# Kernel tuning notes

Measured on AMD Instinct MI355X. Metric: run time of the kernel, lower is better.

## Reference

```python
import jax, jax.numpy as jnp
import numpy as np

N_LOC = 500000
N_CAT = 5000
N_EDGES = 2000000
LOC_DIM = 128
CAT_DIM = 128
INITRANGE = 0.1
NEG_SLOPE = 0.2


def setup_inputs() -> dict:
    key = jax.random.key(0)
    k1, k2, k3, k4 = jax.random.split(key, 4)
    loc_emb = jax.random.normal(k1, (N_LOC, LOC_DIM), dtype=jnp.float32)
    # loc_to_cat Linear params, init per init_weights(): uniform(-0.1, 0.1) weight, zero bias
    W = jax.random.uniform(k2, (CAT_DIM, LOC_DIM), dtype=jnp.float32,
                           minval=-INITRANGE, maxval=INITRANGE)
    b = jnp.zeros((CAT_DIM,), dtype=jnp.float32)
    edge_src = jax.random.randint(k3, (N_EDGES,), 0, N_LOC, dtype=jnp.int64)
    edge_dst = jax.random.randint(k4, (N_EDGES,), 0, N_CAT, dtype=jnp.int64)
    return {"loc_emb": loc_emb, "W": W, "b": b,
            "edge_src": edge_src, "edge_dst": edge_dst}


def reference(loc_emb, W, b, edge_src, edge_dst):
    # copy_u('f','m') + sum('m','in') across all canonical etypes, combined with 'sum':
    # gather source (loc) features along edges, segment-sum into cat nodes.
    msg = loc_emb[edge_src]                                   # [E, loc_dim]
    agg = jax.ops.segment_sum(msg, edge_dst, num_segments=N_CAT)  # [n_cat, loc_dim]
    # loc_to_cat linear + LeakyReLU(0.2)
    cat_emb = jax.nn.leaky_relu(agg @ W.T + b, negative_slope=NEG_SLOPE)
    return cat_emb
```

## Files before the change

kernel.cpp:

```cpp
#include <hip/hip_runtime.h>

#define N_LOC   500000
#define N_CAT   5000
#define N_EDGES 2000000
#define DIM     128
#define NEG_SLOPE 0.2f
#define PAD     5008
#define NB      256
#define EPB     ((N_EDGES + NB - 1) / NB)


__launch_bounds__(1024)
__global__ void blockhist_kernel(const int* __restrict__ edst, int* __restrict__ rank,
                                 int* __restrict__ bhist) {
    __shared__ int lh[N_CAT];
    int b = blockIdx.x, t = threadIdx.x;
    for (int c = t; c < N_CAT; c += 1024) lh[c] = 0;
    __syncthreads();
    int s = b * EPB;
    int e = min(s + EPB, N_EDGES);
    for (int i = s + t; i < e; i += 1024)
        rank[i] = atomicAdd(&lh[edst[i]], 1);
    __syncthreads();
    for (int c = t; c < N_CAT; c += 1024)
        bhist[(size_t)b * N_CAT + c] = lh[c];
}

__launch_bounds__(256)
__global__ void blockscan_kernel(int* __restrict__ bhist, int* __restrict__ tot) {
    int c = blockIdx.x * 256 + threadIdx.x;
    if (c >= N_CAT) return;
    int run = 0;
    for (int b0 = 0; b0 < NB; b0 += 8) {
        int v0 = bhist[(size_t)(b0 + 0) * N_CAT + c];
        int v1 = bhist[(size_t)(b0 + 1) * N_CAT + c];
        int v2 = bhist[(size_t)(b0 + 2) * N_CAT + c];
        int v3 = bhist[(size_t)(b0 + 3) * N_CAT + c];
        int v4 = bhist[(size_t)(b0 + 4) * N_CAT + c];
        int v5 = bhist[(size_t)(b0 + 5) * N_CAT + c];
        int v6 = bhist[(size_t)(b0 + 6) * N_CAT + c];
        int v7 = bhist[(size_t)(b0 + 7) * N_CAT + c];
        bhist[(size_t)(b0 + 0) * N_CAT + c] = run; run += v0;
        bhist[(size_t)(b0 + 1) * N_CAT + c] = run; run += v1;
        bhist[(size_t)(b0 + 2) * N_CAT + c] = run; run += v2;
        bhist[(size_t)(b0 + 3) * N_CAT + c] = run; run += v3;
        bhist[(size_t)(b0 + 4) * N_CAT + c] = run; run += v4;
        bhist[(size_t)(b0 + 5) * N_CAT + c] = run; run += v5;
        bhist[(size_t)(b0 + 6) * N_CAT + c] = run; run += v6;
        bhist[(size_t)(b0 + 7) * N_CAT + c] = run; run += v7;
    }
    tot[c] = run;
}

__launch_bounds__(1024)
__global__ void scan_kernel(const int* __restrict__ cnt, int* __restrict__ offsets) {
    __shared__ int wsum[16];
    __shared__ int woff[16];
    __shared__ int total_s;
    __shared__ int running_s;
    int t = threadIdx.x;
    int lane = t & 63, w = t >> 6;
    if (t == 0) { running_s = 0; offsets[0] = 0; }
    __syncthreads();
    for (int base = 0; base < N_CAT; base += 1024) {
        int i = base + t;
        int v = (i < N_CAT) ? cnt[i] : 0;
        int incl = v;
        #pragma unroll
        for (int off = 1; off < 64; off <<= 1) {
            int x = __shfl_up(incl, off, 64);
            if (lane >= off) incl += x;
        }
        if (lane == 63) wsum[w] = incl;
        __syncthreads();
        if (w == 0 && lane < 16) {
            int s = wsum[lane];
            int e = s;
            #pragma unroll
            for (int off = 1; off < 16; off <<= 1) {
                int x = __shfl_up(e, off, 64);
                if (lane >= off) e += x;
            }
            woff[lane] = e - s;
            if (lane == 15) total_s = e;
        }
        __syncthreads();
        int run = running_s;
        if (i < N_CAT) offsets[i + 1] = run + woff[w] + incl;
        __syncthreads();
        if (t == 0) running_s = run + total_s;
        __syncthreads();
    }
}

__global__ void fill2_kernel(const int* __restrict__ esrc, const int* __restrict__ edst,
                             const int* __restrict__ rank, const int* __restrict__ offsets,
                             const int* __restrict__ bhist, int* __restrict__ csr_src) {
    int i = blockIdx.x * blockDim.x + threadIdx.x;
    if (i < N_EDGES) {
        int c = edst[i];
        int b = i / EPB;
        csr_src[offsets[c] + bhist[(size_t)b * N_CAT + c] + rank[i]] = esrc[i];
    }
}

__global__ void transpose_kernel(const float* __restrict__ W, float* __restrict__ WT) {
    int j = blockIdx.x;
    int k = threadIdx.x;
    WT[k * DIM + j] = W[j * DIM + k];
}

__launch_bounds__(256)
__global__ void agg_fused_kernel(const float* __restrict__ loc, const int* __restrict__ csr_src,
                                 const int* __restrict__ offsets, const float* __restrict__ WT,
                                 const float* __restrict__ bias, float* __restrict__ out) {
    __shared__ float4 sacc[256];
    __shared__ float  srow[DIM];
    int c = blockIdx.x;
    int t = threadIdx.x;
    int g = t >> 5;
    int l = t & 31;
    int beg = offsets[c];
    int end = offsets[c + 1];
    int cnt = end - beg;
    int per = (cnt + 7) >> 3;
    int gbeg = beg + g * per;
    int gend = min(gbeg + per, end);

    float4 a0 = make_float4(0.f, 0.f, 0.f, 0.f);
    float4 a1 = make_float4(0.f, 0.f, 0.f, 0.f);
    float4 a2 = make_float4(0.f, 0.f, 0.f, 0.f);
    float4 a3 = make_float4(0.f, 0.f, 0.f, 0.f);
    int e = gbeg;
    for (; e + 4 <= gend; e += 4) {
        int s0 = csr_src[e + 0];
        int s1 = csr_src[e + 1];
        int s2 = csr_src[e + 2];
        int s3 = csr_src[e + 3];
        float4 v0 = ((const float4*)(loc + (size_t)s0 * DIM))[l];
        float4 v1 = ((const float4*)(loc + (size_t)s1 * DIM))[l];
        float4 v2 = ((const float4*)(loc + (size_t)s2 * DIM))[l];
        float4 v3 = ((const float4*)(loc + (size_t)s3 * DIM))[l];
        a0.x += v0.x; a0.y += v0.y; a0.z += v0.z; a0.w += v0.w;
        a1.x += v1.x; a1.y += v1.y; a1.z += v1.z; a1.w += v1.w;
        a2.x += v2.x; a2.y += v2.y; a2.z += v2.z; a2.w += v2.w;
        a3.x += v3.x; a3.y += v3.y; a3.z += v3.z; a3.w += v3.w;
    }
    for (; e < gend; ++e) {
        int s = csr_src[e];
        float4 v = ((const float4*)(loc + (size_t)s * DIM))[l];
        a0.x += v.x; a0.y += v.y; a0.z += v.z; a0.w += v.w;
    }
    float4 acc = make_float4((a0.x + a1.x) + (a2.x + a3.x),
                             (a0.y + a1.y) + (a2.y + a3.y),
                             (a0.z + a1.z) + (a2.z + a3.z),
                             (a0.w + a1.w) + (a2.w + a3.w));
    sacc[t] = acc;
    __syncthreads();
    if (t < 128) {
        float4 a = sacc[t], b = sacc[t + 128];
        sacc[t] = make_float4(a.x + b.x, a.y + b.y, a.z + b.z, a.w + b.w);
    }
    __syncthreads();
    if (t < 64) {
        float4 a = sacc[t], b = sacc[t + 64];
        sacc[t] = make_float4(a.x + b.x, a.y + b.y, a.z + b.z, a.w + b.w);
    }
    __syncthreads();
    if (t < 32) {
        float4 a = sacc[t], b = sacc[t + 32];
        srow[4 * t + 0] = a.x + b.x;
        srow[4 * t + 1] = a.y + b.y;
        srow[4 * t + 2] = a.z + b.z;
        srow[4 * t + 3] = a.w + b.w;
    }
    __syncthreads();
    int j = t & 127;
    int h = t >> 7;
    float m0 = 0.f, m1 = 0.f, m2 = 0.f, m3 = 0.f;
    int k0 = h * 64;
    #pragma unroll 4
    for (int k = 0; k < 64; k += 4) {
        m0 += WT[(k0 + k + 0) * DIM + j] * srow[k0 + k + 0];
        m1 += WT[(k0 + k + 1) * DIM + j] * srow[k0 + k + 1];
        m2 += WT[(k0 + k + 2) * DIM + j] * srow[k0 + k + 2];
        m3 += WT[(k0 + k + 3) * DIM + j] * srow[k0 + k + 3];
    }
    float* sred = (float*)sacc;
    sred[t] = (m0 + m1) + (m2 + m3);
    __syncthreads();
    if (t < 128) {
        float v = sred[t] + sred[t + 128] + bias[t];
        v = v > 0.f ? v : NEG_SLOPE * v;
        out[(size_t)c * DIM + t] = v;
    }
}


__global__ void hist_rank_kernel(const int* __restrict__ dst, int* __restrict__ cnt,
                                 int* __restrict__ rank, int n) {
    int i = blockIdx.x * blockDim.x + threadIdx.x;
    if (i < n) rank[i] = atomicAdd(&cnt[dst[i]], 1);
}

__global__ void fill_rank_kernel(const int* __restrict__ src, const int* __restrict__ dst,
                                 const int* __restrict__ rank, const int* __restrict__ offsets,
                                 int* __restrict__ csr_src, int n) {
    int i = blockIdx.x * blockDim.x + threadIdx.x;
    if (i < n) csr_src[offsets[dst[i]] + rank[i]] = src[i];
}

__global__ void zero_kernel(float* p, int n) {
    int i = blockIdx.x * blockDim.x + threadIdx.x;
    if (i < n) p[i] = 0.f;
}

__launch_bounds__(128)
__global__ void scatter_atomic_kernel(const float* __restrict__ loc, const int* __restrict__ src,
                                      const int* __restrict__ dst, float* __restrict__ agg) {
    int e = blockIdx.x;
    int d = threadIdx.x;
    int s = src[e];
    int c = dst[e];
    atomicAdd(&agg[(size_t)c * DIM + d], loc[(size_t)s * DIM + d]);
}

#define CATS_PER_BLOCK 8
__launch_bounds__(256)
__global__ void gemm_lrelu_kernel(const float* __restrict__ agg, const float* __restrict__ W,
                                  const float* __restrict__ b, float* __restrict__ out) {
    __shared__ float sW[DIM * 129];
    __shared__ float sA[CATS_PER_BLOCK * DIM];
    int t = threadIdx.x;
    int cbase = blockIdx.x * CATS_PER_BLOCK;
    for (int i = t; i < DIM * DIM; i += 256) {
        int j = i >> 7, k = i & 127;
        sW[j * 129 + k] = W[i];
    }
    for (int i = t; i < CATS_PER_BLOCK * DIM; i += 256) {
        sA[i] = agg[(size_t)cbase * DIM + i];
    }
    __syncthreads();
    int j = t & 127;
    int cc = t >> 7;
    float acc0 = 0.f, acc1 = 0.f, acc2 = 0.f, acc3 = 0.f;
    for (int k = 0; k < DIM; ++k) {
        float w = sW[j * 129 + k];
        acc0 += w * sA[(cc + 0) * DIM + k];
        acc1 += w * sA[(cc + 2) * DIM + k];
        acc2 += w * sA[(cc + 4) * DIM + k];
        acc3 += w * sA[(cc + 6) * DIM + k];
    }
    float bj = b[j];
    float r0 = acc0 + bj, r1 = acc1 + bj, r2 = acc2 + bj, r3 = acc3 + bj;
    r0 = r0 > 0.f ? r0 : NEG_SLOPE * r0;
    r1 = r1 > 0.f ? r1 : NEG_SLOPE * r1;
    r2 = r2 > 0.f ? r2 : NEG_SLOPE * r2;
    r3 = r3 > 0.f ? r3 : NEG_SLOPE * r3;
    out[(size_t)(cbase + cc + 0) * DIM + j] = r0;
    out[(size_t)(cbase + cc + 2) * DIM + j] = r1;
    out[(size_t)(cbase + cc + 4) * DIM + j] = r2;
    out[(size_t)(cbase + cc + 6) * DIM + j] = r3;
}

extern "C" void kernel_launch(void* const* d_in, const int* in_sizes, int n_in,
                              void* d_out, int out_size, void* d_ws, size_t ws_size,
                              hipStream_t stream) {
    const float* loc  = (const float*)d_in[0];
    const float* W    = (const float*)d_in[1];
    const float* bias = (const float*)d_in[2];
    const int*   esrc = (const int*)d_in[3];
    const int*   edst = (const int*)d_in[4];
    float* out = (float*)d_out;

    const int threads = 256;
    const int eblocks = (N_EDGES + threads - 1) / threads;

    size_t need_cs   = ((size_t)2 * N_EDGES + (size_t)NB * N_CAT + 2 * PAD + DIM * DIM) * sizeof(int);
    size_t need_rank = ((size_t)2 * N_EDGES + 2 * PAD + DIM * DIM) * sizeof(int);

    if (ws_size >= need_cs) {
        int*   rank    = (int*)d_ws;
        int*   csr_src = rank + N_EDGES;
        int*   bhist   = csr_src + N_EDGES;
        int*   tot     = bhist + (size_t)NB * N_CAT;
        int*   offsets = tot + PAD;
        float* WT      = (float*)(offsets + PAD);

        transpose_kernel<<<DIM, DIM, 0, stream>>>(W, WT);
        blockhist_kernel<<<NB, 1024, 0, stream>>>(edst, rank, bhist);
        blockscan_kernel<<<(N_CAT + 255) / 256, 256, 0, stream>>>(bhist, tot);
        scan_kernel<<<1, 1024, 0, stream>>>(tot, offsets);
        fill2_kernel<<<eblocks, threads, 0, stream>>>(esrc, edst, rank, offsets, bhist, csr_src);
        agg_fused_kernel<<<N_CAT, 256, 0, stream>>>(loc, csr_src, offsets, WT, bias, out);
    } else if (ws_size >= need_rank) {
        int* counts  = (int*)d_ws;
        int* offsets = counts + PAD;
        float* WT    = (float*)(offsets + PAD);
        int* rank    = (int*)(WT + DIM * DIM);
        int* csr_src = rank + N_EDGES;

        hipMemsetAsync(counts, 0, (size_t)PAD * sizeof(int), stream);
        transpose_kernel<<<DIM, DIM, 0, stream>>>(W, WT);
        hist_rank_kernel<<<eblocks, threads, 0, stream>>>(edst, counts, rank, N_EDGES);
        scan_kernel<<<1, 1024, 0, stream>>>(counts, offsets);
        fill_rank_kernel<<<eblocks, threads, 0, stream>>>(esrc, edst, rank, offsets, csr_src, N_EDGES);
        agg_fused_kernel<<<N_CAT, 256, 0, stream>>>(loc, csr_src, offsets, WT, bias, out);
    } else {
        int n = N_CAT * DIM;
        zero_kernel<<<(n + 255) / 256, 256, 0, stream>>>(out, n);
        scatter_atomic_kernel<<<N_EDGES, DIM, 0, stream>>>(loc, esrc, edst, out);
        gemm_lrelu_kernel<<<N_CAT / CATS_PER_BLOCK, 256, 0, stream>>>(out, W, bias, out);
    }
}
```

Measured before the change: 504.1 us.

## Fuse transpose into histogram, merge block scans, vectorize fill, unroll gather

Reduces the CSR build from five launches to three. The W transpose runs as an extra block of the histogram kernel, and the per-category block-prefix scan and global scan are merged into one single-block kernel that keeps totals in shared memory. The block count drops from 256 to 64, with int4 vectorized histogram and fill loads, and the aggregation gather loop is unrolled to 8 edges to keep more loads in flight. The single-block fused scan now serially walks 64 rows of 5000 entries, and fewer histogram blocks mean less parallelism, which could lengthen the preprocessing critical path.

Result: slower. 519.0 us (+3.0%).

```diff
diff --git a/kernel.cpp b/kernel.cpp
--- a/kernel.cpp
+++ b/kernel.cpp
@@ -6,65 +6,88 @@
 #define DIM     128
 #define NEG_SLOPE 0.2f
 #define PAD     5008
-#define NB      256
-#define EPB     ((N_EDGES + NB - 1) / NB)
-
+#define NB      64
+#define EPB     31252
 
 __launch_bounds__(1024)
-__global__ void blockhist_kernel(const int* __restrict__ edst, int* __restrict__ rank,
+__global__ void blockhist_kernel(const int* __restrict__ edst, const float* __restrict__ W,
+                                 float* __restrict__ WT, int* __restrict__ rank,
                                  int* __restrict__ bhist) {
+    int b = blockIdx.x, t = threadIdx.x;
+    if (b == NB) {
+        for (int i = t; i < DIM * DIM; i += 1024) {
+            int j = i >> 7, k = i & 127;
+            WT[k * DIM + j] = W[j * DIM + k];
+        }
+        return;
+    }
     __shared__ int lh[N_CAT];
-    int b = blockIdx.x, t = threadIdx.x;
     for (int c = t; c < N_CAT; c += 1024) lh[c] = 0;
     __syncthreads();
     int s = b * EPB;
     int e = min(s + EPB, N_EDGES);
-    for (int i = s + t; i < e; i += 1024)
-        rank[i] = atomicAdd(&lh[edst[i]], 1);
+    int i = s + 4 * t;
+    for (; i + 4 <= e; i += 4096) {
+        int4 d = *(const int4*)(edst + i);
+        int4 r;
+        r.x = atomicAdd(&lh[d.x], 1);
+        r.y = atomicAdd(&lh[d.y], 1);
+        r.z = atomicAdd(&lh[d.z], 1);
+        r.w = atomicAdd(&lh[d.w], 1);
+        *(int4*)(rank + i) = r;
+    }
+    if (i < e) {
+        int lim = min(i + 4, e);
+        for (int j = i; j < lim; ++j) rank[j] = atomicAdd(&lh[edst[j]], 1);
+    }
     __syncthreads();
     for (int c = t; c < N_CAT; c += 1024)
         bhist[(size_t)b * N_CAT + c] = lh[c];
 }
 
-__launch_bounds__(256)
-__global__ void blockscan_kernel(int* __restrict__ bhist, int* __restrict__ tot) {
-    int c = blockIdx.x * 256 + threadIdx.x;
-    if (c >= N_CAT) return;
-    int run = 0;
-    for (int b0 = 0; b0 < NB; b0 += 8) {
-        int v0 = bhist[(size_t)(b0 + 0) * N_CAT + c];
-        int v1 = bhist[(size_t)(b0 + 1) * N_CAT + c];
-        int v2 = bhist[(size_t)(b0 + 2) * N_CAT + c];
-        int v3 = bhist[(size_t)(b0 + 3) * N_CAT + c];
-        int v4 = bhist[(size_t)(b0 + 4) * N_CAT + c];
-        int v5 = bhist[(size_t)(b0 + 5) * N_CAT + c];
-        int v6 = bhist[(size_t)(b0 + 6) * N_CAT + c];
-        int v7 = bhist[(size_t)(b0 + 7) * N_CAT + c];
-        bhist[(size_t)(b0 + 0) * N_CAT + c] = run; run += v0;
-        bhist[(size_t)(b0 + 1) * N_CAT + c] = run; run += v1;
-        bhist[(size_t)(b0 + 2) * N_CAT + c] = run; run += v2;
-        bhist[(size_t)(b0 + 3) * N_CAT + c] = run; run += v3;
-        bhist[(size_t)(b0 + 4) * N_CAT + c] = run; run += v4;
-        bhist[(size_t)(b0 + 5) * N_CAT + c] = run; run += v5;
-        bhist[(size_t)(b0 + 6) * N_CAT + c] = run; run += v6;
-        bhist[(size_t)(b0 + 7) * N_CAT + c] = run; run += v7;
-    }
-    tot[c] = run;
-}
-
 __launch_bounds__(1024)
-__global__ void scan_kernel(const int* __restrict__ cnt, int* __restrict__ offsets) {
+__global__ void fused_scan_kernel(int* __restrict__ bhist, int* __restrict__ offsets) {
+    __shared__ int stot[N_CAT];
     __shared__ int wsum[16];
     __shared__ int woff[16];
-    __shared__ int total_s;
-    __shared__ int running_s;
+    __shared__ int total_s, running_s;
     int t = threadIdx.x;
+    int runs[5] = {0, 0, 0, 0, 0};
+    int cur[5], nxt[5];
+    #pragma unroll
+    for (int k = 0; k < 5; ++k) {
+        int c = t + 1024 * k;
+        cur[k] = (c < N_CAT) ? bhist[c] : 0;
+    }
+    for (int b = 0; b < NB; ++b) {
+        size_t base = (size_t)b * N_CAT;
+        if (b + 1 < NB) {
+            size_t nb = base + N_CAT;
+            #pragma unroll
+            for (int k = 0; k < 5; ++k) {
+                int c = t + 1024 * k;
+                nxt[k] = (c < N_CAT) ? bhist[nb + c] : 0;
+            }
+        }
+        #pragma unroll
+        for (int k = 0; k < 5; ++k) {
+            int c = t + 1024 * k;
+            if (c < N_CAT) bhist[base + c] = runs[k];
+            runs[k] += cur[k];
+            cur[k] = nxt[k];
+        }
+    }
+    #pragma unroll
+    for (int k = 0; k < 5; ++k) {
+        int c = t + 1024 * k;
+        if (c < N_CAT) stot[c] = runs[k];
+    }
+    if (t == 0) { running_s = 0; offsets[0] = 0; }
+    __syncthreads();
     int lane = t & 63, w = t >> 6;
-    if (t == 0) { running_s = 0; offsets[0] = 0; }
-    __syncthreads();
-    for (int base = 0; base < N_CAT; base += 1024) {
-        int i = base + t;
-        int v = (i < N_CAT) ? cnt[i] : 0;
+    for (int base2 = 0; base2 < N_CAT; base2 += 1024) {
+        int i2 = base2 + t;
+        int v = (i2 < N_CAT) ? stot[i2] : 0;
         int incl = v;
         #pragma unroll
         for (int off = 1; off < 64; off <<= 1) {
@@ -86,7 +109,7 @@
         }
         __syncthreads();
         int run = running_s;
-        if (i < N_CAT) offsets[i + 1] = run + woff[w] + incl;
+        if (i2 < N_CAT) offsets[i2 + 1] = run + woff[w] + incl;
         __syncthreads();
         if (t == 0) running_s = run + total_s;
         __syncthreads();
@@ -96,18 +119,23 @@
 __global__ void fill2_kernel(const int* __restrict__ esrc, const int* __restrict__ edst,
                              const int* __restrict__ rank, const int* __restrict__ offsets,
                              const int* __restrict__ bhist, int* __restrict__ csr_src) {
-    int i = blockIdx.x * blockDim.x + threadIdx.x;
-    if (i < N_EDGES) {
-        int c = edst[i];
-        int b = i / EPB;
-        csr_src[offsets[c] + bhist[(size_t)b * N_CAT + c] + rank[i]] = esrc[i];
-    }
-}
-
-__global__ void transpose_kernel(const float* __restrict__ W, float* __restrict__ WT) {
-    int j = blockIdx.x;
-    int k = threadIdx.x;
-    WT[k * DIM + j] = W[j * DIM + k];
+    int i4 = (blockIdx.x * blockDim.x + threadIdx.x) * 4;
+    if (i4 + 4 <= N_EDGES) {
+        int4 c = *(const int4*)(edst + i4);
+        int4 s = *(const int4*)(esrc + i4);
+        int4 r = *(const int4*)(rank + i4);
+        size_t bb = (size_t)(i4 / EPB) * N_CAT;
+        csr_src[offsets[c.x] + bhist[bb + c.x] + r.x] = s.x;
+        csr_src[offsets[c.y] + bhist[bb + c.y] + r.y] = s.y;
+        csr_src[offsets[c.z] + bhist[bb + c.z] + r.z] = s.z;
+        csr_src[offsets[c.w] + bhist[bb + c.w] + r.w] = s.w;
+    } else {
+        for (int i = i4; i < N_EDGES; ++i) {
+            int c = edst[i];
+            size_t bb = (size_t)(i / EPB) * N_CAT;
+            csr_src[offsets[c] + bhist[bb + c] + rank[i]] = esrc[i];
+        }
+    }
 }
 
 __launch_bounds__(256)
@@ -132,11 +160,28 @@
     float4 a2 = make_float4(0.f, 0.f, 0.f, 0.f);
     float4 a3 = make_float4(0.f, 0.f, 0.f, 0.f);
     int e = gbeg;
+    for (; e + 8 <= gend; e += 8) {
+        int s0 = csr_src[e + 0], s1 = csr_src[e + 1], s2 = csr_src[e + 2], s3 = csr_src[e + 3];
+        int s4 = csr_src[e + 4], s5 = csr_src[e + 5], s6 = csr_src[e + 6], s7 = csr_src[e + 7];
+        float4 v0 = ((const float4*)(loc + (size_t)s0 * DIM))[l];
+        float4 v1 = ((const float4*)(loc + (size_t)s1 * DIM))[l];
+        float4 v2 = ((const float4*)(loc + (size_t)s2 * DIM))[l];
+        float4 v3 = ((const float4*)(loc + (size_t)s3 * DIM))[l];
+        float4 v4 = ((const float4*)(loc + (size_t)s4 * DIM))[l];
+        float4 v5 = ((const float4*)(loc + (size_t)s5 * DIM))[l];
+        float4 v6 = ((const float4*)(loc + (size_t)s6 * DIM))[l];
+        float4 v7 = ((const float4*)(loc + (size_t)s7 * DIM))[l];
+        a0.x += v0.x; a0.y += v0.y; a0.z += v0.z; a0.w += v0.w;
+        a1.x += v1.x; a1.y += v1.y; a1.z += v1.z; a1.w += v1.w;
+        a2.x += v2.x; a2.y += v2.y; a2.z += v2.z; a2.w += v2.w;
+        a3.x += v3.x; a3.y += v3.y; a3.z += v3.z; a3.w += v3.w;
+        a0.x += v4.x; a0.y += v4.y; a0.z += v4.z; a0.w += v4.w;
+        a1.x += v5.x; a1.y += v5.y; a1.z += v5.z; a1.w += v5.w;
+        a2.x += v6.x; a2.y += v6.y; a2.z += v6.z; a2.w += v6.w;
+        a3.x += v7.x; a3.y += v7.y; a3.z += v7.z; a3.w += v7.w;
+    }
     for (; e + 4 <= gend; e += 4) {
-        int s0 = csr_src[e + 0];
-        int s1 = csr_src[e + 1];
-        int s2 = csr_src[e + 2];
-        int s3 = csr_src[e + 3];
+        int s0 = csr_src[e + 0], s1 = csr_src[e + 1], s2 = csr_src[e + 2], s3 = csr_src[e + 3];
         float4 v0 = ((const float4*)(loc + (size_t)s0 * DIM))[l];
         float4 v1 = ((const float4*)(loc + (size_t)s1 * DIM))[l];
         float4 v2 = ((const float4*)(loc + (size_t)s2 * DIM))[l];
@@ -210,6 +255,52 @@
     if (i < n) csr_src[offsets[dst[i]] + rank[i]] = src[i];
 }
 
+__launch_bounds__(1024)
+__global__ void scan_kernel(const int* __restrict__ cnt, int* __restrict__ offsets) {
+    __shared__ int wsum[16];
+    __shared__ int woff[16];
+    __shared__ int total_s, running_s;
+    int t = threadIdx.x;
+    int lane = t & 63, w = t >> 6;
+    if (t == 0) { running_s = 0; offsets[0] = 0; }
+    __syncthreads();
+    for (int base = 0; base < N_CAT; base += 1024) {
+        int i = base + t;
+        int v = (i < N_CAT) ? cnt[i] : 0;
+        int incl = v;
+        #pragma unroll
+        for (int off = 1; off < 64; off <<= 1) {
+            int x = __shfl_up(incl, off, 64);
+            if (lane >= off) incl += x;
+        }
+        if (lane == 63) wsum[w] = incl;
+        __syncthreads();
+        if (w == 0 && lane < 16) {
+            int s = wsum[lane];
+            int e = s;
+            #pragma unroll
+            for (int off = 1; off < 16; off <<= 1) {
+                int x = __shfl_up(e, off, 64);
+                if (lane >= off) e += x;
+            }
+            woff[lane] = e - s;
+            if (lane == 15) total_s = e;
+        }
+        __syncthreads();
+        int run = running_s;
+        if (i < N_CAT) offsets[i + 1] = run + woff[w] + incl;
+        __syncthreads();
+        if (t == 0) running_s = run + total_s;
+        __syncthreads();
+    }
+}
+
+__global__ void transpose_kernel(const float* __restrict__ W, float* __restrict__ WT) {
+    int j = blockIdx.x;
+    int k = threadIdx.x;
+    WT[k * DIM + j] = W[j * DIM + k];
+}
+
 __global__ void zero_kernel(float* p, int n) {
     int i = blockIdx.x * blockDim.x + threadIdx.x;
     if (i < n) p[i] = 0.f;
@@ -220,9 +311,7 @@
                                       const int* __restrict__ dst, float* __restrict__ agg) {
     int e = blockIdx.x;
     int d = threadIdx.x;
-    int s = src[e];
-    int c = dst[e];
-    atomicAdd(&agg[(size_t)c * DIM + d], loc[(size_t)s * DIM + d]);
+    atomicAdd(&agg[(size_t)dst[e] * DIM + d], loc[(size_t)src[e] * DIM + d]);
 }
 
 #define CATS_PER_BLOCK 8
@@ -237,9 +326,8 @@
         int j = i >> 7, k = i & 127;
         sW[j * 129 + k] = W[i];
     }
-    for (int i = t; i < CATS_PER_BLOCK * DIM; i += 256) {
+    for (int i = t; i < CATS_PER_BLOCK * DIM; i += 256)
         sA[i] = agg[(size_t)cbase * DIM + i];
-    }
     __syncthreads();
     int j = t & 127;
     int cc = t >> 7;
@@ -273,9 +361,6 @@
     const int*   edst = (const int*)d_in[4];
     float* out = (float*)d_out;
 
-    const int threads = 256;
-    const int eblocks = (N_EDGES + threads - 1) / threads;
-
     size_t need_cs   = ((size_t)2 * N_EDGES + (size_t)NB * N_CAT + 2 * PAD + DIM * DIM) * sizeof(int);
     size_t need_rank = ((size_t)2 * N_EDGES + 2 * PAD + DIM * DIM) * sizeof(int);
 
@@ -283,15 +368,12 @@
         int*   rank    = (int*)d_ws;
         int*   csr_src = rank + N_EDGES;
         int*   bhist   = csr_src + N_EDGES;
-        int*   tot     = bhist + (size_t)NB * N_CAT;
-        int*   offsets = tot + PAD;
+        int*   offsets = bhist + (size_t)NB * N_CAT;
         float* WT      = (float*)(offsets + PAD);
 
-        transpose_kernel<<<DIM, DIM, 0, stream>>>(W, WT);
-        blockhist_kernel<<<NB, 1024, 0, stream>>>(edst, rank, bhist);
-        blockscan_kernel<<<(N_CAT + 255) / 256, 256, 0, stream>>>(bhist, tot);
-        scan_kernel<<<1, 1024, 0, stream>>>(tot, offsets);
-        fill2_kernel<<<eblocks, threads, 0, stream>>>(esrc, edst, rank, offsets, bhist, csr_src);
+        blockhist_kernel<<<NB + 1, 1024, 0, stream>>>(edst, W, WT, rank, bhist);
+        fused_scan_kernel<<<1, 1024, 0, stream>>>(bhist, offsets);
+        fill2_kernel<<<(N_EDGES / 4 + 255) / 256, 256, 0, stream>>>(esrc, edst, rank, offsets, bhist, csr_src);
         agg_fused_kernel<<<N_CAT, 256, 0, stream>>>(loc, csr_src, offsets, WT, bias, out);
     } else if (ws_size >= need_rank) {
         int* counts  = (int*)d_ws;
@@ -302,9 +384,10 @@
 
         hipMemsetAsync(counts, 0, (size_t)PAD * sizeof(int), stream);
         transpose_kernel<<<DIM, DIM, 0, stream>>>(W, WT);
-        hist_rank_kernel<<<eblocks, threads, 0, stream>>>(edst, counts, rank, N_EDGES);
+        const int eblocks = (N_EDGES + 255) / 256;
+        hist_rank_kernel<<<eblocks, 256, 0, stream>>>(edst, counts, rank, N_EDGES);
         scan_kernel<<<1, 1024, 0, stream>>>(counts, offsets);
-        fill_rank_kernel<<<eblocks, threads, 0, stream>>>(esrc, edst, rank, offsets, csr_src, N_EDGES);
+        fill_rank_kernel<<<eblocks, 256, 0, stream>>>(esrc, edst, rank, offsets, csr_src, N_EDGES);
         agg_fused_kernel<<<N_CAT, 256, 0, stream>>>(loc, csr_src, offsets, WT, bias, out);
     } else {
         int n = N_CAT * DIM;
```
